# Kernel optimization log

Hardware: AMD Instinct MI355X
Metric: run time of the kernel (lower is better)

The kernel has to match this reference:

```python
import jax, jax.numpy as jnp
import numpy as np

H = 8          # heads
KP = 6         # num_sparse keypoint tokens per group
NUM_PATCHES = 256


def _build_mask(N, Nk):
    # mask_q: [H, 3, N] bool, query token (g=0, i=0) disabled
    mask_q = np.ones((H, 3, N), dtype=bool)
    mask_q[:, 0, 0] = False
    # mask_k: [H, 3, Nk] bool, key token j=0 disabled for all groups
    mask_k = np.ones((H, 3, Nk), dtype=bool)
    mask_k[:, :, 0] = False
    keep = mask_q[:, :, :, None] & mask_k[:, :, None, :]  # [H,3,N,Nk]
    return jnp.asarray(~keep)  # True where masked out


def setup_inputs() -> dict:
    key = jax.random.key(0)
    k1, k2, k3 = jax.random.split(key, 3)
    B, G, N, D = 64, 3, NUM_PATCHES + KP, 512
    x = jax.random.normal(k1, (B, G, N, D), dtype=jnp.float32)
    w_qkv = jax.random.normal(k2, (D, 3 * D), dtype=jnp.float32) * (D ** -0.5)
    w_out = jax.random.normal(k3, (D, D), dtype=jnp.float32) * (D ** -0.5)
    b_out = jnp.zeros((D,), dtype=jnp.float32)
    return {"x": x, "w_qkv": w_qkv, "w_out": w_out, "b_out": b_out}


def reference(x, w_qkv, w_out, b_out):
    B, G, N, D = x.shape
    Dh = D // H
    scale = D ** -0.5  # scale_with_head=False

    qkv = x @ w_qkv  # [B,G,N,3D]
    q, k, v = jnp.split(qkv, 3, axis=-1)

    def to_heads(t):  # b g n (h d) -> b h g n d
        return t.reshape(B, G, N, H, Dh).transpose(0, 3, 1, 2, 4)

    q, k, v = to_heads(q), to_heads(k), to_heads(v)

    # gather keypoint K/V from all groups, shared across every group
    k_kp = k[:, :, :, :KP].reshape(B, H, 1, G * KP, Dh)
    v_kp = v[:, :, :, :KP].reshape(B, H, 1, G * KP, Dh)
    k_kp = jnp.broadcast_to(k_kp, (B, H, G, G * KP, Dh))
    v_kp = jnp.broadcast_to(v_kp, (B, H, G, G * KP, Dh))
    k = jnp.concatenate([k_kp, k[:, :, :, KP:]], axis=3)  # [B,H,G,Nk,Dh]
    v = jnp.concatenate([v_kp, v[:, :, :, KP:]], axis=3)
    Nk = k.shape[3]

    dots = jnp.einsum('bhgid,bhgjd->bhgij', q, k) * scale
    masked = _build_mask(N, Nk)  # [H,3,N,Nk], broadcasts over B
    neg = -jnp.finfo(dots.dtype).max
    dots = jnp.where(masked[None], neg, dots)

    attn = jax.nn.softmax(dots, axis=-1)
    out = jnp.einsum('bhgij,bhgjd->bhgid', attn, v)
    out = out.transpose(0, 2, 3, 1, 4).reshape(B, G, N, D)  # b h g n d -> b g n (h d)
    out = out @ w_out + b_out
    return out, dots
```

## Files before the change

kernel.cpp:

```cpp
#include <hip/hip_runtime.h>
#include <float.h>
#include <math.h>

#define B_   64
#define G_   3
#define N_   262
#define D_   512
#define H_   8
#define DH   64
#define KP_  6
#define NKP  18
#define NK   274
#define TD3  1536
#define M_   50304
#define SCALE 0.044194173824159216f
#define LOG2E 1.4426950408889634f

typedef unsigned short u16;
typedef __attribute__((ext_vector_type(4))) float f32x4;
typedef __attribute__((ext_vector_type(2))) float f32x2;
typedef float f32x4u __attribute__((ext_vector_type(4), aligned(4)));
typedef __attribute__((ext_vector_type(8))) short bf16x8;

__device__ __forceinline__ u16 f2bf(float f) {
    unsigned int u = __float_as_uint(f);
    u += 0x7FFFu + ((u >> 16) & 1u);
    return (u16)(u >> 16);
}
__device__ __forceinline__ unsigned pack2bf(float lo, float hi) {
    unsigned ul = __float_as_uint(lo); ul += 0x7FFFu + ((ul >> 16) & 1u);
    unsigned uh = __float_as_uint(hi); uh += 0x7FFFu + ((uh >> 16) & 1u);
    return (ul >> 16) | (uh & 0xFFFF0000u);
}
__device__ __forceinline__ float mask_val() { return __uint_as_float(0xFF7F0000u); }

__device__ __forceinline__ void gload16(const void* g, void* l) {
    __builtin_amdgcn_global_load_lds(
        (const __attribute__((address_space(1))) unsigned int*)g,
        (__attribute__((address_space(3))) unsigned int*)l, 16, 0, 0);
}

__global__ __launch_bounds__(256)
void cast4(const float* __restrict__ in, u16* __restrict__ o, int n4)
{
    int i = blockIdx.x * 256 + threadIdx.x;
    if (i < n4) {
        float4 v = ((const float4*)in)[i];
        u16 r[4] = { f2bf(v.x), f2bf(v.y), f2bf(v.z), f2bf(v.w) };
        *(uint2*)(o + (size_t)i * 4) = *(uint2*)r;
    }
}

__global__ __launch_bounds__(256)
void tcast(const float* __restrict__ w, u16* __restrict__ wT, int K, int N)
{
    int idx = blockIdx.x * 256 + threadIdx.x;
    if (idx < K * N) {
        int nn = idx / K, kk = idx - nn * K;
        wT[idx] = f2bf(w[(size_t)kk * N + nn]);
    }
}

template<int OUT_BF16>
__global__ __launch_bounds__(512)
void gemm_bf16(const u16* __restrict__ A, const u16* __restrict__ WT,
               float* __restrict__ Cf, u16* __restrict__ Cb,
               const float* __restrict__ bias, int Ndim, int Kdim)
{
    __shared__ u16 Asm[128 * 64];
    __shared__ u16 Bsm[256 * 64];

    const int tid  = threadIdx.x;
    const int lane = tid & 63;
    const int wid  = tid >> 6;
    const int l15  = lane & 15;
    const int lg   = lane >> 4;
    const int wr   = (wid & 1) * 64;
    const int wc   = (wid >> 1) * 64;
    const int row0 = blockIdx.y * 128;
    const int col0 = blockIdx.x * 256;

    const u16* srcA[2];
    #pragma unroll
    for (int i = 0; i < 2; ++i) {
        int slot = i * 512 + tid;
        int r = slot >> 3;
        int sblk = (slot & 7) ^ (r & 7);
        srcA[i] = A + (size_t)(row0 + r) * Kdim + sblk * 8;
    }
    const u16* srcB[4];
    #pragma unroll
    for (int i = 0; i < 4; ++i) {
        int slot = i * 512 + tid;
        int r = slot >> 3;
        int sblk = (slot & 7) ^ (r & 7);
        srcB[i] = WT + (size_t)(col0 + r) * Kdim + sblk * 8;
    }

    f32x4 acc[4][4] = {};

    for (int k0 = 0; k0 < Kdim; k0 += 64) {
        #pragma unroll
        for (int i = 0; i < 2; ++i)
            gload16(srcA[i] + k0, &Asm[(i * 512 + wid * 64) * 8]);
        #pragma unroll
        for (int i = 0; i < 4; ++i)
            gload16(srcB[i] + k0, &Bsm[(i * 512 + wid * 64) * 8]);
        __syncthreads();
        #pragma unroll
        for (int kk = 0; kk < 2; ++kk) {
            const int xb = (kk * 4 + lg) ^ (l15 & 7);
            bf16x8 a[4], b[4];
            #pragma unroll
            for (int m = 0; m < 4; ++m) a[m] = *(const bf16x8*)&Asm[(wr + m * 16 + l15) * 64 + xb * 8];
            #pragma unroll
            for (int n = 0; n < 4; ++n) b[n] = *(const bf16x8*)&Bsm[(wc + n * 16 + l15) * 64 + xb * 8];
            #pragma unroll
            for (int m = 0; m < 4; ++m)
                #pragma unroll
                for (int n = 0; n < 4; ++n)
                    acc[m][n] = __builtin_amdgcn_mfma_f32_16x16x32_bf16(a[m], b[n], acc[m][n], 0, 0, 0);
        }
        __syncthreads();
    }

    const int rbase = row0 + wr + lg * 4;
    const int cbase = col0 + wc + l15;
    #pragma unroll
    for (int m = 0; m < 4; ++m)
        #pragma unroll
        for (int n = 0; n < 4; ++n) {
            const int col = cbase + n * 16;
            #pragma unroll
            for (int r = 0; r < 4; ++r) {
                const int row = rbase + m * 16 + r;
                float v = acc[m][n][r];
                if (OUT_BF16) Cb[(size_t)row * Ndim + col] = f2bf(v);
                else          Cf[(size_t)row * Ndim + col] = v + bias[col];
            }
        }
}

__global__ __launch_bounds__(512, 1)
void attn_bf16(const u16* __restrict__ qkv, float* __restrict__ dots,
               u16* __restrict__ otmp)
{
    __shared__ u16 Ks[288 * 72];
    __shared__ u16 Vt[64 * 296];
    __shared__ float rowbuf[8][8 * 276];

    const int tid  = threadIdx.x;
    const int lane = tid & 63;
    const int wid  = tid >> 6;
    const int l15  = lane & 15;
    const int lg   = lane >> 4;

    const int bhg = blockIdx.x;
    const int b   = bhg / (H_ * G_);
    const int h   = (bhg / G_) % H_;
    const int g   = bhg % G_;
    const int rowbase = (b * G_ + g) * N_;
    const size_t dbase0 = (((size_t)(b * H_ + h) * G_ + g) * N_) * NK;

    for (int it = 0; it < 5; ++it) {
        int lin = tid + it * 512;
        if (lin < 2304) {
            int tok = lin >> 3, kg = (lin & 7) << 3;
            uint4 kv = make_uint4(0, 0, 0, 0), vv = make_uint4(0, 0, 0, 0);
            if (tok < NK) {
                int gs, ns;
                if (tok < NKP) { gs = tok / KP_; ns = tok - gs * KP_; }
                else           { gs = g;         ns = tok - NKP + KP_; }
                const u16* p = qkv + ((size_t)((b * G_ + gs) * N_ + ns)) * TD3 + h * DH + kg;
                kv = *(const uint4*)(p + D_);
                vv = *(const uint4*)(p + 2 * D_);
            }
            *(uint4*)&Ks[tok * 72 + kg] = kv;
            int slot = ((tok >> 5) << 5) | (((tok & 15) >> 2) << 3) | (((tok >> 4) & 1) << 2) | (tok & 3);
            union { uint4 u4; u16 us[8]; } u; u.u4 = vv;
            #pragma unroll
            for (int e = 0; e < 8; ++e) Vt[(kg + e) * 296 + slot] = u.us[e];
        }
    }
    __syncthreads();

    float* rb = rowbuf[wid];

    for (int t = wid; t < 17; t += 8) {
        const int n0 = t * 16;
        int qrow = n0 + l15; if (qrow > N_ - 1) qrow = N_ - 1;
        const u16* qp = qkv + (size_t)(rowbase + qrow) * TD3 + h * DH;
        bf16x8 qa0 = *(const bf16x8*)(qp + lg * 8);
        bf16x8 qa1 = *(const bf16x8*)(qp + 32 + lg * 8);

        f32x4 c[18];
        __builtin_amdgcn_s_setprio(1);
        #pragma unroll
        for (int jt = 0; jt < 18; ++jt) {
            const u16* kr = &Ks[(jt * 16 + l15) * 72];
            bf16x8 kb0 = *(const bf16x8*)(kr + lg * 8);
            bf16x8 kb1 = *(const bf16x8*)(kr + 32 + lg * 8);
            f32x4 z = {};
            z = __builtin_amdgcn_mfma_f32_16x16x32_bf16(kb0, qa0, z, 0, 0, 0);
            c[jt] = __builtin_amdgcn_mfma_f32_16x16x32_bf16(kb1, qa1, z, 0, 0, 0);
        }
        __builtin_amdgcn_s_setprio(0);

        #pragma unroll
        for (int jt = 0; jt < 18; ++jt)
            #pragma unroll
            for (int rr = 0; rr < 4; ++rr) c[jt][rr] *= SCALE;
        c[0][0] = (lg == 0) ? mask_val() : c[0][0];
        if (g == 0 && t == 0) {
            #pragma unroll
            for (int jt = 0; jt < 18; ++jt)
                #pragma unroll
                for (int rr = 0; rr < 4; ++rr)
                    c[jt][rr] = (l15 == 0) ? mask_val() : c[jt][rr];
        }

        const int ph_of_lane = l15 >> 3;
        const int r8 = l15 & 7;
        #pragma unroll
        for (int ph = 0; ph < 2; ++ph) {
            if (ph_of_lane == ph) {
                float* rr_ = &rb[r8 * 276];
                #pragma unroll
                for (int jt = 0; jt < 17; ++jt)
                    *(f32x4*)&rr_[jt * 16 + 4 * lg] = c[jt];
                if (lg == 0) { f32x2 tl = { c[17][0], c[17][1] }; *(f32x2*)&rr_[272] = tl; }
            }
            const int base_row = n0 + 8 * ph;
            const size_t base_f = dbase0 + (size_t)base_row * NK;
            #pragma unroll
            for (int r = 0; r < 8; ++r) {
                if (base_row + r < N_) {
                    const float* rrb = &rb[r * 276];
                    float* gp = &dots[base_f + (size_t)r * NK];
                    #pragma unroll
                    for (int i2 = 0; i2 < 2; ++i2) {
                        int ch = lane + (i2 << 6);
                        if (ch < 68) {
                            f32x4 v = *(const f32x4*)&rrb[ch * 4];
                            *(f32x4u*)&gp[ch * 4] = v;
                        } else if (ch == 68) {
                            f32x2 v2 = *(const f32x2*)&rrb[272];
                            *(f32x2*)&gp[272] = v2;
                        }
                    }
                }
            }
        }

        c[17][2] = -INFINITY; c[17][3] = -INFINITY;
        c[17][0] = (lg == 0) ? c[17][0] : -INFINITY;
        c[17][1] = (lg == 0) ? c[17][1] : -INFINITY;

        float mx = c[0][0];
        #pragma unroll
        for (int jt = 0; jt < 18; ++jt)
            #pragma unroll
            for (int rr = 0; rr < 4; ++rr) mx = fmaxf(mx, c[jt][rr]);
        mx = fmaxf(mx, __shfl_xor(mx, 16, 64));
        mx = fmaxf(mx, __shfl_xor(mx, 32, 64));
        float s = 0.f;
        #pragma unroll
        for (int jt = 0; jt < 18; ++jt)
            #pragma unroll
            for (int rr = 0; rr < 4; ++rr) {
                float p = exp2f((c[jt][rr] - mx) * LOG2E);
                c[jt][rr] = p;
                s += p;
            }
        s += __shfl_xor(s, 16, 64);
        s += __shfl_xor(s, 32, 64);
        const float inv = 1.f / s;

        f32x4 o[4] = {};
        __builtin_amdgcn_s_setprio(1);
        #pragma unroll
        for (int sl = 0; sl < 9; ++sl) {
            union { bf16x8 v; unsigned u[4]; } pa;
            pa.u[0] = pack2bf(c[2 * sl][0],     c[2 * sl][1]);
            pa.u[1] = pack2bf(c[2 * sl][2],     c[2 * sl][3]);
            pa.u[2] = pack2bf(c[2 * sl + 1][0], c[2 * sl + 1][1]);
            pa.u[3] = pack2bf(c[2 * sl + 1][2], c[2 * sl + 1][3]);
            #pragma unroll
            for (int dt = 0; dt < 4; ++dt) {
                bf16x8 vb = *(const bf16x8*)&Vt[(dt * 16 + l15) * 296 + sl * 32 + lg * 8];
                o[dt] = __builtin_amdgcn_mfma_f32_16x16x32_bf16(pa.v, vb, o[dt], 0, 0, 0);
            }
        }
        __builtin_amdgcn_s_setprio(0);

        u16* ob = (u16*)rb;
        #pragma unroll
        for (int dt = 0; dt < 4; ++dt)
            #pragma unroll
            for (int rr = 0; rr < 4; ++rr) {
                const int q = lg * 4 + rr;
                const float iq = __shfl(inv, q, 64);
                ob[q * 64 + dt * 16 + l15] = f2bf(o[dt][rr] * iq);
            }
        {
            const int vrows = min(16, N_ - n0);
            const int nch = vrows * 8;
            #pragma unroll
            for (int i2 = 0; i2 < 2; ++i2) {
                int ch = lane + (i2 << 6);
                if (ch < nch) {
                    int r = ch >> 3, cp = ch & 7;
                    uint4 v = *(const uint4*)&ob[ch * 8];
                    *(uint4*)(otmp + (size_t)(rowbase + n0 + r) * D_ + h * DH + cp * 8) = v;
                }
            }
        }
    }
}

extern "C" void kernel_launch(void* const* d_in, const int* in_sizes, int n_in,
                              void* d_out, int out_size, void* d_ws, size_t ws_size,
                              hipStream_t stream)
{
    const float* x     = (const float*)d_in[0];
    const float* w_qkv = (const float*)d_in[1];
    const float* w_out = (const float*)d_in[2];
    const float* b_out = (const float*)d_in[3];

    float* out  = (float*)d_out;
    float* dots = out + (size_t)M_ * D_;

    u16* xb    = (u16*)d_ws;
    u16* wqkvT = xb    + (size_t)M_ * D_;
    u16* woutT = wqkvT + (size_t)TD3 * D_;
    u16* qkvb  = woutT + (size_t)D_ * D_;
    u16* otmpb = qkvb  + (size_t)M_ * TD3;

    cast4<<<(M_ * D_ / 4 + 255) / 256, 256, 0, stream>>>(x, xb, M_ * D_ / 4);
    tcast<<<(TD3 * D_ + 255) / 256, 256, 0, stream>>>(w_qkv, wqkvT, D_, TD3);
    tcast<<<(D_ * D_ + 255) / 256, 256, 0, stream>>>(w_out, woutT, D_, D_);

    gemm_bf16<1><<<dim3(TD3 / 256, M_ / 128), 512, 0, stream>>>(
        xb, wqkvT, nullptr, qkvb, nullptr, TD3, D_);

    attn_bf16<<<dim3(B_ * H_ * G_), 512, 0, stream>>>(qkvb, dots, otmpb);

    gemm_bf16<0><<<dim3(D_ / 256, M_ / 128), 512, 0, stream>>>(
        otmpb, woutT, out, nullptr, b_out, D_, D_);
}
```

Before: 374.5 us.

## Write V transposed from QKV GEMM and read K/V directly from global in attention

The QKV GEMM epilogue now writes the V columns in a per-head transposed layout (head-dim major, token contiguous) through a shared-memory staging tile, instead of the row-major bf16 output. The attention kernel drops its large K and V shared-memory staging. It reads K fragments straight from the global qkv buffer and V fragments from the transposed buffer, keeping only a small LDS tile for the keypoint and tail slices. With much less LDS the launch bounds rise to 4 blocks per CU, trading LDS reuse for more global/L2 traffic and higher occupancy. The setprio hints are also removed.

```diff
diff --git a/kernel.cpp b/kernel.cpp
--- a/kernel.cpp
+++ b/kernel.cpp
@@ -61,14 +61,16 @@
     }
 }
 
-template<int OUT_BF16>
+template<int MODE>
 __global__ __launch_bounds__(512)
 void gemm_bf16(const u16* __restrict__ A, const u16* __restrict__ WT,
                float* __restrict__ Cf, u16* __restrict__ Cb,
+               u16* __restrict__ vws,
                const float* __restrict__ bias, int Ndim, int Kdim)
 {
-    __shared__ u16 Asm[128 * 64];
-    __shared__ u16 Bsm[256 * 64];
+    __shared__ u16 smem[128 * 64 + 256 * 64];
+    u16* Asm = smem;
+    u16* Bsm = smem + 128 * 64;
 
     const int tid  = threadIdx.x;
     const int lane = tid & 63;
@@ -124,6 +126,35 @@
         __syncthreads();
     }
 
+    if (MODE == 1 && col0 >= 1024) {
+        const int h = (col0 - 1024 + wc) >> 6;
+        u16* tls = smem + wid * 2560;
+        const int tok0 = row0 + wr;
+        #pragma unroll
+        for (int p = 0; p < 2; ++p) {
+            #pragma unroll
+            for (int mh = 0; mh < 2; ++mh) {
+                const int m = 2 * p + mh;
+                #pragma unroll
+                for (int n = 0; n < 4; ++n) {
+                    const int d = n * 16 + l15;
+                    #pragma unroll
+                    for (int r = 0; r < 4; ++r) {
+                        const int tl = lg * 4 + mh * 16 + r;
+                        tls[d * 40 + tl] = f2bf(acc[m][n][r]);
+                    }
+                }
+            }
+            #pragma unroll
+            for (int dd = 0; dd < 4; ++dd) {
+                const int d = dd * 16 + l15;
+                uint4 v = *(const uint4*)&tls[d * 40 + lg * 8];
+                *(uint4*)(vws + (size_t)(h * 64 + d) * M_ + tok0 + p * 32 + lg * 8) = v;
+            }
+        }
+        return;
+    }
+
     const int rbase = row0 + wr + lg * 4;
     const int cbase = col0 + wc + l15;
     #pragma unroll
@@ -135,19 +166,18 @@
             for (int r = 0; r < 4; ++r) {
                 const int row = rbase + m * 16 + r;
                 float v = acc[m][n][r];
-                if (OUT_BF16) Cb[(size_t)row * Ndim + col] = f2bf(v);
-                else          Cf[(size_t)row * Ndim + col] = v + bias[col];
-            }
-        }
-}
-
-__global__ __launch_bounds__(512, 1)
-void attn_bf16(const u16* __restrict__ qkv, float* __restrict__ dots,
-               u16* __restrict__ otmp)
-{
-    __shared__ u16 Ks[288 * 72];
-    __shared__ u16 Vt[64 * 296];
+                if (MODE == 1) Cb[(size_t)row * Ndim + col] = f2bf(v);
+                else           Cf[(size_t)row * Ndim + col] = v + bias[col];
+            }
+        }
+}
+
+__global__ __launch_bounds__(512, 4)
+void attn_bf16(const u16* __restrict__ qkv, const u16* __restrict__ vws,
+               float* __restrict__ dots, u16* __restrict__ otmp)
+{
     __shared__ float rowbuf[8][8 * 276];
+    __shared__ u16 Vt0[64 * 72];
 
     const int tid  = threadIdx.x;
     const int lane = tid & 63;
@@ -162,28 +192,21 @@
     const int rowbase = (b * G_ + g) * N_;
     const size_t dbase0 = (((size_t)(b * H_ + h) * G_ + g) * N_) * NK;
 
-    for (int it = 0; it < 5; ++it) {
-        int lin = tid + it * 512;
-        if (lin < 2304) {
-            int tok = lin >> 3, kg = (lin & 7) << 3;
-            uint4 kv = make_uint4(0, 0, 0, 0), vv = make_uint4(0, 0, 0, 0);
-            if (tok < NK) {
-                int gs, ns;
-                if (tok < NKP) { gs = tok / KP_; ns = tok - gs * KP_; }
-                else           { gs = g;         ns = tok - NKP + KP_; }
-                const u16* p = qkv + ((size_t)((b * G_ + gs) * N_ + ns)) * TD3 + h * DH + kg;
-                kv = *(const uint4*)(p + D_);
-                vv = *(const uint4*)(p + 2 * D_);
-            }
-            *(uint4*)&Ks[tok * 72 + kg] = kv;
-            int slot = ((tok >> 5) << 5) | (((tok & 15) >> 2) << 3) | (((tok >> 4) & 1) << 2) | (tok & 3);
-            union { uint4 u4; u16 us[8]; } u; u.u4 = vv;
-            #pragma unroll
-            for (int e = 0; e < 8; ++e) Vt[(kg + e) * 296 + slot] = u.us[e];
-        }
+    for (int idx = tid; idx < 64 * 64; idx += 512) {
+        int s = idx & 63, d = idx >> 6;
+        int key = (s < 32) ? s : (224 + s);
+        u16 v = 0;
+        if (key < NK) {
+            int gs, ns;
+            if (key < NKP) { gs = key / KP_; ns = key - gs * KP_; }
+            else           { gs = g;         ns = key - (NKP - KP_); }
+            v = vws[(size_t)(h * 64 + d) * M_ + (size_t)((b * G_ + gs) * N_ + ns)];
+        }
+        Vt0[d * 72 + s] = v;
     }
     __syncthreads();
 
+    const u16* kbase = qkv + (size_t)(rowbase - (NKP - KP_)) * TD3 + D_ + h * DH + lg * 8;
     float* rb = rowbuf[wid];
 
     for (int t = wid; t < 17; t += 8) {
@@ -194,17 +217,26 @@
         bf16x8 qa1 = *(const bf16x8*)(qp + 32 + lg * 8);
 
         f32x4 c[18];
-        __builtin_amdgcn_s_setprio(1);
         #pragma unroll
         for (int jt = 0; jt < 18; ++jt) {
-            const u16* kr = &Ks[(jt * 16 + l15) * 72];
-            bf16x8 kb0 = *(const bf16x8*)(kr + lg * 8);
-            bf16x8 kb1 = *(const bf16x8*)(kr + 32 + lg * 8);
+            const u16* kp;
+            if (jt >= 2) {
+                int tok = jt * 16 + l15;
+                if (jt == 17 && l15 >= 2) tok = NKP;
+                kp = kbase + (size_t)tok * TD3;
+            } else {
+                int tok = jt * 16 + l15;
+                int gs = (tok * 171) >> 10;
+                int row = (tok < NKP) ? ((b * G_ + gs) * N_ + (tok - gs * KP_))
+                                      : (rowbase + tok - (NKP - KP_));
+                kp = qkv + (size_t)row * TD3 + D_ + h * DH + lg * 8;
+            }
+            bf16x8 kb0 = *(const bf16x8*)kp;
+            bf16x8 kb1 = *(const bf16x8*)(kp + 32);
             f32x4 z = {};
             z = __builtin_amdgcn_mfma_f32_16x16x32_bf16(kb0, qa0, z, 0, 0, 0);
             c[jt] = __builtin_amdgcn_mfma_f32_16x16x32_bf16(kb1, qa1, z, 0, 0, 0);
         }
-        __builtin_amdgcn_s_setprio(0);
 
         #pragma unroll
         for (int jt = 0; jt < 18; ++jt)
@@ -277,7 +309,6 @@
         const float inv = 1.f / s;
 
         f32x4 o[4] = {};
-        __builtin_amdgcn_s_setprio(1);
         #pragma unroll
         for (int sl = 0; sl < 9; ++sl) {
             union { bf16x8 v; unsigned u[4]; } pa;
@@ -287,11 +318,22 @@
             pa.u[3] = pack2bf(c[2 * sl + 1][2], c[2 * sl + 1][3]);
             #pragma unroll
             for (int dt = 0; dt < 4; ++dt) {
-                bf16x8 vb = *(const bf16x8*)&Vt[(dt * 16 + l15) * 296 + sl * 32 + lg * 8];
-                o[dt] = __builtin_amdgcn_mfma_f32_16x16x32_bf16(pa.v, vb, o[dt], 0, 0, 0);
-            }
-        }
-        __builtin_amdgcn_s_setprio(0);
+                union { bf16x8 v; uint2 u2[2]; unsigned u[4]; } vb;
+                if (sl == 0 || sl == 8) {
+                    const int sb = (sl == 8) ? 32 : 0;
+                    vb.u2[0] = *(const uint2*)&Vt0[(dt * 16 + l15) * 72 + sb + 4 * lg];
+                    vb.u2[1] = *(const uint2*)&Vt0[(dt * 16 + l15) * 72 + sb + 16 + 4 * lg];
+                } else {
+                    const u16* vr = vws + (size_t)(h * 64 + dt * 16 + l15) * M_
+                                  + (rowbase - (NKP - KP_)) + sl * 32 + 4 * lg;
+                    vb.u[0] = *(const unsigned*)(vr);
+                    vb.u[1] = *(const unsigned*)(vr + 2);
+                    vb.u[2] = *(const unsigned*)(vr + 16);
+                    vb.u[3] = *(const unsigned*)(vr + 18);
+                }
+                o[dt] = __builtin_amdgcn_mfma_f32_16x16x32_bf16(pa.v, vb.v, o[dt], 0, 0, 0);
+            }
+        }
 
         u16* ob = (u16*)rb;
         #pragma unroll
@@ -334,17 +376,18 @@
     u16* wqkvT = xb    + (size_t)M_ * D_;
     u16* woutT = wqkvT + (size_t)TD3 * D_;
     u16* qkvb  = woutT + (size_t)D_ * D_;
-    u16* otmpb = qkvb  + (size_t)M_ * TD3;
+    u16* vws   = qkvb  + (size_t)M_ * TD3;
+    u16* otmpb = vws   + (size_t)8 * 64 * M_;
 
     cast4<<<(M_ * D_ / 4 + 255) / 256, 256, 0, stream>>>(x, xb, M_ * D_ / 4);
     tcast<<<(TD3 * D_ + 255) / 256, 256, 0, stream>>>(w_qkv, wqkvT, D_, TD3);
     tcast<<<(D_ * D_ + 255) / 256, 256, 0, stream>>>(w_out, woutT, D_, D_);
 
     gemm_bf16<1><<<dim3(TD3 / 256, M_ / 128), 512, 0, stream>>>(
-        xb, wqkvT, nullptr, qkvb, nullptr, TD3, D_);
-
-    attn_bf16<<<dim3(B_ * H_ * G_), 512, 0, stream>>>(qkvb, dots, otmpb);
+        xb, wqkvT, nullptr, qkvb, vws, nullptr, TD3, D_);
+
+    attn_bf16<<<dim3(B_ * H_ * G_), 512, 0, stream>>>(qkvb, vws, dots, otmpb);
 
     gemm_bf16<0><<<dim3(D_ / 256, M_ / 128), 512, 0, stream>>>(
-        otmpb, woutT, out, nullptr, b_out, D_, D_);
-}
+        otmpb, woutT, out, nullptr, nullptr, b_out, D_, D_);
+}
```

Result: slower. 982.1 us (+162.3%).
